# Kernel tuning notes

Hardware: AMD Instinct MI355X
Metric: run time of the kernel (lower is better)

Reference implementation:

```python
import jax, jax.numpy as jnp
import numpy as np

B, S, D = 64, 2048, 512

def setup_inputs() -> dict:
    key = jax.random.key(0)
    ks = jax.random.split(key, 7)
    return {
        "sent_vec": jax.random.normal(ks[0], (B, S, D), dtype=jnp.float32),
        "c1_vec": jax.random.normal(ks[1], (B, D), dtype=jnp.float32),
        "c2_vec": jax.random.normal(ks[2], (B, D), dtype=jnp.float32),
        "c3_vec": jax.random.normal(ks[3], (B, D), dtype=jnp.float32),
        "c4_vec": jax.random.normal(ks[4], (B, D), dtype=jnp.float32),
        "kernel": jax.random.normal(ks[5], (D, D), dtype=jnp.float32) * 0.05,
        "bias": jax.random.normal(ks[6], (D, 1), dtype=jnp.float32) * 0.05,
    }

def reference(sent_vec, c1_vec, c2_vec, c3_vec, c4_vec, kernel, bias):
    # Wh: [B,S,D], bh: [B,S]
    Wh = jnp.einsum("bsd,de->bse", sent_vec, kernel)
    bh = jnp.einsum("bsd,do->bs", sent_vec, bias)  # bias is [D,1]
    c = jnp.stack([c1_vec, c2_vec, c3_vec, c4_vec], axis=0)  # [4,B,D]
    # scores: [4,B,S] = Wh . u + bh, softmax over seq axis
    scores = jnp.einsum("bse,cbe->cbs", Wh, c) + bh[None]
    attn = jax.nn.softmax(scores, axis=-1)
    # weighted sum over seq: [4,B,D]
    P = jnp.einsum("cbs,bsd->cbd", attn, sent_vec)
    return (P[0], P[1], P[2], P[3])
```

## Files before the change

### kernel.cpp

```cpp
#include <hip/hip_runtime.h>
#include <hip/hip_bf16.h>
#include <math.h>

constexpr int B = 64;
constexpr int S = 2048;
constexpr int D = 512;
constexpr int NCHUNK = 8;
constexpr int CHUNK = S / NCHUNK;
constexpr int NW = 4;
constexpr int ROWS_PER_WAVE = CHUNK / NW;
constexpr int NGRP = ROWS_PER_WAVE / 4;
constexpr int NPART = NCHUNK;

__global__ __launch_bounds__(256) void compute_v_kernel(
    const float* __restrict__ K, const float* __restrict__ bias,
    const float* __restrict__ c1, const float* __restrict__ c2,
    const float* __restrict__ c3, const float* __restrict__ c4,
    float* __restrict__ v)
{
    const int b = blockIdx.y;
    const int dchunk = blockIdx.x;
    __shared__ float c_lds[4][D];

    const float* cptr0 = c1 + (size_t)b * D;
    const float* cptr1 = c2 + (size_t)b * D;
    const float* cptr2 = c3 + (size_t)b * D;
    const float* cptr3 = c4 + (size_t)b * D;
    for (int i = threadIdx.x; i < D; i += 256) {
        c_lds[0][i] = cptr0[i];
        c_lds[1][i] = cptr1[i];
        c_lds[2][i] = cptr2[i];
        c_lds[3][i] = cptr3[i];
    }
    __syncthreads();

    const int wave = threadIdx.x >> 6;
    const int lane = threadIdx.x & 63;

    #pragma unroll
    for (int r = 0; r < 16; ++r) {
        const int d = dchunk * 64 + wave * 16 + r;
        const float* krow = K + (size_t)d * D;
        float a0 = 0.f, a1 = 0.f, a2 = 0.f, a3 = 0.f;
        #pragma unroll
        for (int k = 0; k < D / 64; ++k) {
            const float kv = krow[k * 64 + lane];
            a0 = fmaf(kv, c_lds[0][k * 64 + lane], a0);
            a1 = fmaf(kv, c_lds[1][k * 64 + lane], a1);
            a2 = fmaf(kv, c_lds[2][k * 64 + lane], a2);
            a3 = fmaf(kv, c_lds[3][k * 64 + lane], a3);
        }
        float u  = (lane & 1) ? a1 : a0;
        float uo = (lane & 1) ? a0 : a1;
        u += __shfl_xor(uo, 1);
        float w_ = (lane & 1) ? a3 : a2;
        float wo = (lane & 1) ? a2 : a3;
        w_ += __shfl_xor(wo, 1);
        float p  = (lane & 2) ? w_ : u;
        float q  = (lane & 2) ? u : w_;
        p += __shfl_xor(q, 2);
        p += __shfl_xor(p, 4);
        p += __shfl_xor(p, 8);
        p += __shfl_xor(p, 16);
        p += __shfl_xor(p, 32);
        if (lane < 4)
            v[((size_t)lane * B + b) * D + d] = p + bias[d];
    }
}

__global__ __launch_bounds__(256) void flash_kernel(
    const float* __restrict__ sent, const float* __restrict__ v,
    float* __restrict__ partML, float* __restrict__ partP)
{
    const int b = blockIdx.y;
    const int ch = blockIdx.x;
    const int t = threadIdx.x;
    const int wave = t >> 6;
    const int lane = t & 63;

    __shared__ float p_lds[NW][4][D];
    __shared__ float ml_lds[NW][4][2];

    float vlo[4][4], vhi[4][4];
    #pragma unroll
    for (int c = 0; c < 4; ++c) {
        const float4 lo = *(const float4*)&v[((size_t)c * B + b) * D + lane * 4];
        const float4 hi = *(const float4*)&v[((size_t)c * B + b) * D + 256 + lane * 4];
        vlo[c][0] = lo.x; vlo[c][1] = lo.y; vlo[c][2] = lo.z; vlo[c][3] = lo.w;
        vhi[c][0] = hi.x; vhi[c][1] = hi.y; vhi[c][2] = hi.z; vhi[c][3] = hi.w;
    }

    const size_t sbase = ((size_t)b * S + (size_t)ch * CHUNK + (size_t)wave * ROWS_PER_WAVE) * D;

    float m = -INFINITY, lsum = 0.f;
    float plo[4][4] = {{0}}, phi[4][4] = {{0}};

    float xA[4][8], xB[4][8];

    auto loadg = [&](float (&x)[4][8], int g) {
        const float* src = sent + sbase + (size_t)g * 4 * D + lane * 4;
        #pragma unroll
        for (int rr = 0; rr < 4; ++rr) {
            const float4 lo = *(const float4*)(src + rr * D);
            const float4 hi = *(const float4*)(src + rr * D + 256);
            x[rr][0] = lo.x; x[rr][1] = lo.y; x[rr][2] = lo.z; x[rr][3] = lo.w;
            x[rr][4] = hi.x; x[rr][5] = hi.y; x[rr][6] = hi.z; x[rr][7] = hi.w;
        }
    };

    auto compute = [&](float (&x)[4][8]) {
        float s[4];
        #pragma unroll
        for (int rr = 0; rr < 4; ++rr) {
            float a0 = 0.f, a1 = 0.f, a2 = 0.f, a3 = 0.f;
            #pragma unroll
            for (int j = 0; j < 4; ++j) {
                a0 = fmaf(x[rr][j], vlo[0][j], a0); a0 = fmaf(x[rr][4 + j], vhi[0][j], a0);
                a1 = fmaf(x[rr][j], vlo[1][j], a1); a1 = fmaf(x[rr][4 + j], vhi[1][j], a1);
                a2 = fmaf(x[rr][j], vlo[2][j], a2); a2 = fmaf(x[rr][4 + j], vhi[2][j], a2);
                a3 = fmaf(x[rr][j], vlo[3][j], a3); a3 = fmaf(x[rr][4 + j], vhi[3][j], a3);
            }
            float u  = (lane & 1) ? a1 : a0;
            float uo = (lane & 1) ? a0 : a1;
            u += __shfl_xor(uo, 1);
            float w_ = (lane & 1) ? a3 : a2;
            float wo = (lane & 1) ? a2 : a3;
            w_ += __shfl_xor(wo, 1);
            float p  = (lane & 2) ? w_ : u;
            float q  = (lane & 2) ? u : w_;
            p += __shfl_xor(q, 2);
            p += __shfl_xor(p, 4);
            p += __shfl_xor(p, 8);
            p += __shfl_xor(p, 16);
            p += __shfl_xor(p, 32);
            s[rr] = p;
        }

        const float tm = fmaxf(fmaxf(s[0], s[1]), fmaxf(s[2], s[3]));
        if (!__all(tm <= m)) {
            const float mn = fmaxf(m, tm);
            const float cr = __expf(m - mn);
            m = mn;
            lsum *= cr;
            #pragma unroll
            for (int c = 0; c < 4; ++c) {
                const float crc = __int_as_float(__builtin_amdgcn_readlane(__float_as_int(cr), c));
                #pragma unroll
                for (int j = 0; j < 4; ++j) { plo[c][j] *= crc; phi[c][j] *= crc; }
            }
        }
        float w4[4];
        #pragma unroll
        for (int rr = 0; rr < 4; ++rr) { w4[rr] = __expf(s[rr] - m); lsum += w4[rr]; }

        #pragma unroll
        for (int rr = 0; rr < 4; ++rr) {
            #pragma unroll
            for (int c = 0; c < 4; ++c) {
                const float wc = __int_as_float(__builtin_amdgcn_readlane(__float_as_int(w4[rr]), c));
                plo[c][0] = fmaf(wc, x[rr][0], plo[c][0]);
                plo[c][1] = fmaf(wc, x[rr][1], plo[c][1]);
                plo[c][2] = fmaf(wc, x[rr][2], plo[c][2]);
                plo[c][3] = fmaf(wc, x[rr][3], plo[c][3]);
                phi[c][0] = fmaf(wc, x[rr][4], phi[c][0]);
                phi[c][1] = fmaf(wc, x[rr][5], phi[c][1]);
                phi[c][2] = fmaf(wc, x[rr][6], phi[c][2]);
                phi[c][3] = fmaf(wc, x[rr][7], phi[c][3]);
            }
        }
    };

    loadg(xA, 0);
    for (int g = 0; g < NGRP; g += 2) {
        loadg(xB, g + 1);
        compute(xA);
        if (g + 2 < NGRP) loadg(xA, g + 2);
        compute(xB);
    }

    #pragma unroll
    for (int c = 0; c < 4; ++c) {
        *(float4*)&p_lds[wave][c][lane * 4] =
            make_float4(plo[c][0], plo[c][1], plo[c][2], plo[c][3]);
        *(float4*)&p_lds[wave][c][256 + lane * 4] =
            make_float4(phi[c][0], phi[c][1], phi[c][2], phi[c][3]);
    }
    if (lane < 4) { ml_lds[wave][lane][0] = m; ml_lds[wave][lane][1] = lsum; }
    __syncthreads();

    {
        const int c = wave;
        float mi0 = ml_lds[0][c][0], mi1 = ml_lds[1][c][0];
        float mi2 = ml_lds[2][c][0], mi3 = ml_lds[3][c][0];
        const float mg = fmaxf(fmaxf(mi0, mi1), fmaxf(mi2, mi3));
        const float e0 = __expf(mi0 - mg), e1 = __expf(mi1 - mg);
        const float e2 = __expf(mi2 - mg), e3 = __expf(mi3 - mg);
        const float lg = e0 * ml_lds[0][c][1] + e1 * ml_lds[1][c][1]
                       + e2 * ml_lds[2][c][1] + e3 * ml_lds[3][c][1];

        float4 aLo = make_float4(0.f, 0.f, 0.f, 0.f);
        float4 aHi = make_float4(0.f, 0.f, 0.f, 0.f);
        const float ee[1] = {0};  (void)ee;
        {
            const float4 q0 = *(const float4*)&p_lds[0][c][lane * 4];
            const float4 q1 = *(const float4*)&p_lds[1][c][lane * 4];
            const float4 q2 = *(const float4*)&p_lds[2][c][lane * 4];
            const float4 q3 = *(const float4*)&p_lds[3][c][lane * 4];
            aLo.x = e0*q0.x + e1*q1.x + e2*q2.x + e3*q3.x;
            aLo.y = e0*q0.y + e1*q1.y + e2*q2.y + e3*q3.y;
            aLo.z = e0*q0.z + e1*q1.z + e2*q2.z + e3*q3.z;
            aLo.w = e0*q0.w + e1*q1.w + e2*q2.w + e3*q3.w;
            const float4 r0 = *(const float4*)&p_lds[0][c][256 + lane * 4];
            const float4 r1 = *(const float4*)&p_lds[1][c][256 + lane * 4];
            const float4 r2 = *(const float4*)&p_lds[2][c][256 + lane * 4];
            const float4 r3 = *(const float4*)&p_lds[3][c][256 + lane * 4];
            aHi.x = e0*r0.x + e1*r1.x + e2*r2.x + e3*r3.x;
            aHi.y = e0*r0.y + e1*r1.y + e2*r2.y + e3*r3.y;
            aHi.z = e0*r0.z + e1*r1.z + e2*r2.z + e3*r3.z;
            aHi.w = e0*r0.w + e1*r1.w + e2*r2.w + e3*r3.w;
        }

        const size_t pb = (size_t)(b * NCHUNK + ch) * 4 + c;
        *(float4*)&partP[pb * D + lane * 4] = aLo;
        *(float4*)&partP[pb * D + 256 + lane * 4] = aHi;
        if (lane == 0) {
            partML[pb * 2 + 0] = mg;
            partML[pb * 2 + 1] = lg;
        }
    }
}

__global__ __launch_bounds__(128) void combine_kernel(
    const float* __restrict__ partML, const float* __restrict__ partP,
    float* __restrict__ out)
{
    const int c = blockIdx.x & 3;
    const int b = blockIdx.x >> 2;
    const int t = threadIdx.x;

    float mg = -INFINITY;
    #pragma unroll
    for (int i = 0; i < NPART; ++i)
        mg = fmaxf(mg, partML[((size_t)(b * NCHUNK + i) * 4 + c) * 2 + 0]);

    float lg = 0.f;
    float4 acc = make_float4(0.f, 0.f, 0.f, 0.f);
    #pragma unroll
    for (int i = 0; i < NPART; ++i) {
        const size_t pb = (size_t)(b * NCHUNK + i) * 4 + c;
        const float mi = partML[pb * 2 + 0];
        const float li = partML[pb * 2 + 1];
        const float sc = __expf(mi - mg);
        lg += sc * li;
        const float4 p = *(const float4*)&partP[pb * D + t * 4];
        acc.x = fmaf(sc, p.x, acc.x);
        acc.y = fmaf(sc, p.y, acc.y);
        acc.z = fmaf(sc, p.z, acc.z);
        acc.w = fmaf(sc, p.w, acc.w);
    }
    const float inv = 1.f / lg;
    acc.x *= inv; acc.y *= inv; acc.z *= inv; acc.w *= inv;
    *(float4*)&out[((size_t)c * B + b) * D + t * 4] = acc;
}

extern "C" void kernel_launch(void* const* d_in, const int* in_sizes, int n_in,
                              void* d_out, int out_size, void* d_ws, size_t ws_size,
                              hipStream_t stream)
{
    const float* sent = (const float*)d_in[0];
    const float* c1   = (const float*)d_in[1];
    const float* c2   = (const float*)d_in[2];
    const float* c3   = (const float*)d_in[3];
    const float* c4   = (const float*)d_in[4];
    const float* K    = (const float*)d_in[5];
    const float* bias = (const float*)d_in[6];
    float* out = (float*)d_out;

    float* v      = (float*)d_ws;
    float* partML = (float*)((char*)d_ws + 4 * B * D * 4);
    float* partP  = (float*)((char*)d_ws + 4 * B * D * 4
                             + B * NCHUNK * 4 * 2 * 4);

    compute_v_kernel<<<dim3(8, B), 256, 0, stream>>>(K, bias, c1, c2, c3, c4, v);
    flash_kernel<<<dim3(NCHUNK, B), 256, 0, stream>>>(sent, v, partML, partP);
    combine_kernel<<<4 * B, 128, 0, stream>>>(partML, partP, out);
}
```

Before: 67.25 us.

## Fuse split-softmax combine into flash kernel via last-block ticket and double chunks

Removes the separate combine kernel: each flash block takes an atomic ticket per batch, and the last block to finish merges all partial max/sum/P results and writes the output. The sequence split is also doubled to 16 chunks, giving 1024 blocks instead of 512 for better occupancy across CUs. The cost is one extra atomic and fence per block, a serialized tail merge in one block per batch, and twice as many partials to read back.

```diff
diff --git a/kernel.cpp b/kernel.cpp
--- a/kernel.cpp
+++ b/kernel.cpp
@@ -5,22 +5,23 @@
 constexpr int B = 64;
 constexpr int S = 2048;
 constexpr int D = 512;
-constexpr int NCHUNK = 8;
+constexpr int NCHUNK = 16;
 constexpr int CHUNK = S / NCHUNK;
 constexpr int NW = 4;
 constexpr int ROWS_PER_WAVE = CHUNK / NW;
 constexpr int NGRP = ROWS_PER_WAVE / 4;
-constexpr int NPART = NCHUNK;
 
 __global__ __launch_bounds__(256) void compute_v_kernel(
     const float* __restrict__ K, const float* __restrict__ bias,
     const float* __restrict__ c1, const float* __restrict__ c2,
     const float* __restrict__ c3, const float* __restrict__ c4,
-    float* __restrict__ v)
+    float* __restrict__ v, int* __restrict__ cnt)
 {
     const int b = blockIdx.y;
     const int dchunk = blockIdx.x;
     __shared__ float c_lds[4][D];
+
+    if (blockIdx.x == 0 && threadIdx.x == 0) cnt[b] = 0;
 
     const float* cptr0 = c1 + (size_t)b * D;
     const float* cptr1 = c2 + (size_t)b * D;
@@ -70,7 +71,8 @@
 
 __global__ __launch_bounds__(256) void flash_kernel(
     const float* __restrict__ sent, const float* __restrict__ v,
-    float* __restrict__ partML, float* __restrict__ partP)
+    float* __restrict__ partML, float* __restrict__ partP,
+    int* __restrict__ cnt, float* __restrict__ out)
 {
     const int b = blockIdx.y;
     const int ch = blockIdx.x;
@@ -80,6 +82,7 @@
 
     __shared__ float p_lds[NW][4][D];
     __shared__ float ml_lds[NW][4][2];
+    __shared__ int ticket_s;
 
     float vlo[4][4], vhi[4][4];
     #pragma unroll
@@ -190,35 +193,32 @@
 
     {
         const int c = wave;
-        float mi0 = ml_lds[0][c][0], mi1 = ml_lds[1][c][0];
-        float mi2 = ml_lds[2][c][0], mi3 = ml_lds[3][c][0];
+        const float mi0 = ml_lds[0][c][0], mi1 = ml_lds[1][c][0];
+        const float mi2 = ml_lds[2][c][0], mi3 = ml_lds[3][c][0];
         const float mg = fmaxf(fmaxf(mi0, mi1), fmaxf(mi2, mi3));
         const float e0 = __expf(mi0 - mg), e1 = __expf(mi1 - mg);
         const float e2 = __expf(mi2 - mg), e3 = __expf(mi3 - mg);
         const float lg = e0 * ml_lds[0][c][1] + e1 * ml_lds[1][c][1]
                        + e2 * ml_lds[2][c][1] + e3 * ml_lds[3][c][1];
 
-        float4 aLo = make_float4(0.f, 0.f, 0.f, 0.f);
-        float4 aHi = make_float4(0.f, 0.f, 0.f, 0.f);
-        const float ee[1] = {0};  (void)ee;
-        {
-            const float4 q0 = *(const float4*)&p_lds[0][c][lane * 4];
-            const float4 q1 = *(const float4*)&p_lds[1][c][lane * 4];
-            const float4 q2 = *(const float4*)&p_lds[2][c][lane * 4];
-            const float4 q3 = *(const float4*)&p_lds[3][c][lane * 4];
-            aLo.x = e0*q0.x + e1*q1.x + e2*q2.x + e3*q3.x;
-            aLo.y = e0*q0.y + e1*q1.y + e2*q2.y + e3*q3.y;
-            aLo.z = e0*q0.z + e1*q1.z + e2*q2.z + e3*q3.z;
-            aLo.w = e0*q0.w + e1*q1.w + e2*q2.w + e3*q3.w;
-            const float4 r0 = *(const float4*)&p_lds[0][c][256 + lane * 4];
-            const float4 r1 = *(const float4*)&p_lds[1][c][256 + lane * 4];
-            const float4 r2 = *(const float4*)&p_lds[2][c][256 + lane * 4];
-            const float4 r3 = *(const float4*)&p_lds[3][c][256 + lane * 4];
-            aHi.x = e0*r0.x + e1*r1.x + e2*r2.x + e3*r3.x;
-            aHi.y = e0*r0.y + e1*r1.y + e2*r2.y + e3*r3.y;
-            aHi.z = e0*r0.z + e1*r1.z + e2*r2.z + e3*r3.z;
-            aHi.w = e0*r0.w + e1*r1.w + e2*r2.w + e3*r3.w;
-        }
+        const float4 q0 = *(const float4*)&p_lds[0][c][lane * 4];
+        const float4 q1 = *(const float4*)&p_lds[1][c][lane * 4];
+        const float4 q2 = *(const float4*)&p_lds[2][c][lane * 4];
+        const float4 q3 = *(const float4*)&p_lds[3][c][lane * 4];
+        float4 aLo;
+        aLo.x = e0*q0.x + e1*q1.x + e2*q2.x + e3*q3.x;
+        aLo.y = e0*q0.y + e1*q1.y + e2*q2.y + e3*q3.y;
+        aLo.z = e0*q0.z + e1*q1.z + e2*q2.z + e3*q3.z;
+        aLo.w = e0*q0.w + e1*q1.w + e2*q2.w + e3*q3.w;
+        const float4 r0 = *(const float4*)&p_lds[0][c][256 + lane * 4];
+        const float4 r1 = *(const float4*)&p_lds[1][c][256 + lane * 4];
+        const float4 r2 = *(const float4*)&p_lds[2][c][256 + lane * 4];
+        const float4 r3 = *(const float4*)&p_lds[3][c][256 + lane * 4];
+        float4 aHi;
+        aHi.x = e0*r0.x + e1*r1.x + e2*r2.x + e3*r3.x;
+        aHi.y = e0*r0.y + e1*r1.y + e2*r2.y + e3*r3.y;
+        aHi.z = e0*r0.z + e1*r1.z + e2*r2.z + e3*r3.z;
+        aHi.w = e0*r0.w + e1*r1.w + e2*r2.w + e3*r3.w;
 
         const size_t pb = (size_t)(b * NCHUNK + ch) * 4 + c;
         *(float4*)&partP[pb * D + lane * 4] = aLo;
@@ -228,39 +228,47 @@
             partML[pb * 2 + 1] = lg;
         }
     }
-}
-
-__global__ __launch_bounds__(128) void combine_kernel(
-    const float* __restrict__ partML, const float* __restrict__ partP,
-    float* __restrict__ out)
-{
-    const int c = blockIdx.x & 3;
-    const int b = blockIdx.x >> 2;
-    const int t = threadIdx.x;
-
-    float mg = -INFINITY;
-    #pragma unroll
-    for (int i = 0; i < NPART; ++i)
-        mg = fmaxf(mg, partML[((size_t)(b * NCHUNK + i) * 4 + c) * 2 + 0]);
-
-    float lg = 0.f;
-    float4 acc = make_float4(0.f, 0.f, 0.f, 0.f);
-    #pragma unroll
-    for (int i = 0; i < NPART; ++i) {
-        const size_t pb = (size_t)(b * NCHUNK + i) * 4 + c;
-        const float mi = partML[pb * 2 + 0];
-        const float li = partML[pb * 2 + 1];
-        const float sc = __expf(mi - mg);
-        lg += sc * li;
-        const float4 p = *(const float4*)&partP[pb * D + t * 4];
-        acc.x = fmaf(sc, p.x, acc.x);
-        acc.y = fmaf(sc, p.y, acc.y);
-        acc.z = fmaf(sc, p.z, acc.z);
-        acc.w = fmaf(sc, p.w, acc.w);
-    }
-    const float inv = 1.f / lg;
-    acc.x *= inv; acc.y *= inv; acc.z *= inv; acc.w *= inv;
-    *(float4*)&out[((size_t)c * B + b) * D + t * 4] = acc;
+
+    __threadfence();
+    if (t == 0) ticket_s = atomicAdd(&cnt[b], 1);
+    __syncthreads();
+    if (ticket_s != NCHUNK - 1) return;
+    __threadfence();
+
+    {
+        const int c = wave;
+        float mg = -INFINITY;
+        #pragma unroll
+        for (int i = 0; i < NCHUNK; ++i)
+            mg = fmaxf(mg, partML[((size_t)(b * NCHUNK + i) * 4 + c) * 2 + 0]);
+
+        float lg = 0.f;
+        float4 accLo = make_float4(0.f, 0.f, 0.f, 0.f);
+        float4 accHi = make_float4(0.f, 0.f, 0.f, 0.f);
+        #pragma unroll
+        for (int i = 0; i < NCHUNK; ++i) {
+            const size_t pb = (size_t)(b * NCHUNK + i) * 4 + c;
+            const float mi = partML[pb * 2 + 0];
+            const float li = partML[pb * 2 + 1];
+            const float sc = __expf(mi - mg);
+            lg += sc * li;
+            const float4 p = *(const float4*)&partP[pb * D + lane * 4];
+            accLo.x = fmaf(sc, p.x, accLo.x);
+            accLo.y = fmaf(sc, p.y, accLo.y);
+            accLo.z = fmaf(sc, p.z, accLo.z);
+            accLo.w = fmaf(sc, p.w, accLo.w);
+            const float4 q = *(const float4*)&partP[pb * D + 256 + lane * 4];
+            accHi.x = fmaf(sc, q.x, accHi.x);
+            accHi.y = fmaf(sc, q.y, accHi.y);
+            accHi.z = fmaf(sc, q.z, accHi.z);
+            accHi.w = fmaf(sc, q.w, accHi.w);
+        }
+        const float inv = 1.f / lg;
+        accLo.x *= inv; accLo.y *= inv; accLo.z *= inv; accLo.w *= inv;
+        accHi.x *= inv; accHi.y *= inv; accHi.z *= inv; accHi.w *= inv;
+        *(float4*)&out[((size_t)c * B + b) * D + lane * 4] = accLo;
+        *(float4*)&out[((size_t)c * B + b) * D + 256 + lane * 4] = accHi;
+    }
 }
 
 extern "C" void kernel_launch(void* const* d_in, const int* in_sizes, int n_in,
@@ -276,12 +284,12 @@
     const float* bias = (const float*)d_in[6];
     float* out = (float*)d_out;
 
-    float* v      = (float*)d_ws;
-    float* partML = (float*)((char*)d_ws + 4 * B * D * 4);
-    float* partP  = (float*)((char*)d_ws + 4 * B * D * 4
-                             + B * NCHUNK * 4 * 2 * 4);
-
-    compute_v_kernel<<<dim3(8, B), 256, 0, stream>>>(K, bias, c1, c2, c3, c4, v);
-    flash_kernel<<<dim3(NCHUNK, B), 256, 0, stream>>>(sent, v, partML, partP);
-    combine_kernel<<<4 * B, 128, 0, stream>>>(partML, partP, out);
+    char* ws = (char*)d_ws;
+    float* v      = (float*)ws;                         ws += 4 * B * D * 4;
+    int*   cnt    = (int*)ws;                           ws += 4096;
+    float* partML = (float*)ws;                         ws += B * NCHUNK * 4 * 2 * 4;
+    float* partP  = (float*)ws;
+
+    compute_v_kernel<<<dim3(8, B), 256, 0, stream>>>(K, bias, c1, c2, c3, c4, v, cnt);
+    flash_kernel<<<dim3(NCHUNK, B), 256, 0, stream>>>(sent, v, partML, partP, cnt, out);
 }
```

Measured after the change: 254.6 us. 3.79x slower.
